# Kernel tuning notes

Hardware: AMD Instinct MI355X
Metric: run time of the kernel (lower is better)

## Reference

```python
import jax, jax.numpy as jnp
import numpy as np


def setup_inputs() -> dict:
    key = jax.random.key(0)
    ks = jax.random.split(key, 8)
    B, H, W = 4, 1024, 1024
    F_, Nuv = 40000, 25000
    Ht, Wt = 1024, 1024
    # pytorch3d-style globally packed face indices: pixel of batch b holds idx in [b*F, (b+1)*F) or -1
    local = jax.random.randint(ks[0], (B, H, W, 1), 0, F_)
    covered = jax.random.uniform(ks[1], (B, H, W, 1)) < 0.8
    offset = (jnp.arange(B) * F_)[:, None, None, None]
    pix_to_face = jnp.where(covered, local + offset, -1).astype(jnp.int64)
    bary = jax.random.uniform(ks[2], (B, H, W, 1, 3), dtype=jnp.float32)
    bary = bary / jnp.sum(bary, axis=-1, keepdims=True)
    uvmap = jax.random.normal(ks[3], (B, 3, Ht, Wt), dtype=jnp.float32)
    vertex_uv = jax.random.uniform(ks[4], (Nuv, 2), dtype=jnp.float32)
    face_uv = jax.random.randint(ks[5], (F_, 3), 0, Nuv).astype(jnp.int64)
    bkg_color = jnp.zeros((3,), jnp.float32)
    return {"bary_coords": bary, "uvmap": uvmap, "vertex_uv": vertex_uv,
            "bkg_color": bkg_color, "pix_to_face": pix_to_face,
            "face_uv": face_uv, "num_faces": F_}


def _bilinear_sample(tex, u, v):
    # tex: [B,C,Ht,Wt]; u,v: [B,H,W] in pixel coords (align_corners=True), border padding
    B, C, Ht, Wt = tex.shape
    u = jnp.clip(u, 0.0, Wt - 1.0)
    v = jnp.clip(v, 0.0, Ht - 1.0)
    x0 = jnp.floor(u)
    y0 = jnp.floor(v)
    x0i = x0.astype(jnp.int32)
    y0i = y0.astype(jnp.int32)
    x1i = jnp.minimum(x0i + 1, Wt - 1)
    y1i = jnp.minimum(y0i + 1, Ht - 1)
    wx = (u - x0)[..., None]
    wy = (v - y0)[..., None]
    bidx = jnp.arange(B)[:, None, None]
    g = lambda yi, xi: tex[bidx, :, yi, xi]  # [B,H,W,C]
    top = g(y0i, x0i) * (1.0 - wx) + g(y0i, x1i) * wx
    bot = g(y1i, x0i) * (1.0 - wx) + g(y1i, x1i) * wx
    return top * (1.0 - wy) + bot * wy  # [B,H,W,C]


def reference(bary_coords, uvmap, vertex_uv, bkg_color, pix_to_face, face_uv, num_faces):
    B, H, W, K = pix_to_face.shape
    Ht, Wt = uvmap.shape[2], uvmap.shape[3]
    # vertex_uv with v flipped, as in forward(): stack((u, 1-v))
    vt = jnp.stack([vertex_uv[:, 0], 1.0 - vertex_uv[:, 1]], axis=1)  # [Nuv,2]
    face_vt = vt[face_uv]  # [F,3,2]
    pf = pix_to_face[..., 0]  # [B,H,W] globally packed indices
    valid = pf != -1
    # unpack global -> per-batch local face index (invalid pixels -> 0, masked later)
    local = jnp.where(valid, pf - jnp.arange(B, dtype=pf.dtype)[:, None, None] * num_faces, 0)
    uv_tri = face_vt[local]  # [B,H,W,3,2]
    # barycentric interpolation of the 3 vertex uvs
    uv = jnp.einsum('bhwk,bhwkc->bhwc', bary_coords[:, :, :, 0, :], uv_tri)  # [B,H,W,2]
    sampled = _bilinear_sample(uvmap, uv[..., 0] * (Wt - 1), uv[..., 1] * (Ht - 1))  # [B,H,W,3]
    render = jnp.transpose(sampled, (0, 3, 1, 2))  # [B,3,H,W]
    is_valid = valid[:, None, :, :].astype(render.dtype)  # [B,1,H,W]
    render = render * is_valid + bkg_color[None, :, None, None] * (1.0 - is_valid)
    return render, is_valid
```

## Files before the change

### kernel.cpp

```cpp
#include <hip/hip_runtime.h>
#include <hip/hip_fp16.h>


#define BB   4
#define HWT  (1 << 20)
#define WMASK 1023

static __device__ __forceinline__ unsigned h2b(float a, float b) {
    __half2 h = __floats2half2_rn(a, b);
    return *reinterpret_cast<const unsigned*>(&h);
}
static __device__ __forceinline__ float2 h2f(unsigned u) {
    return __half22float2(*reinterpret_cast<const __half2*>(&u));
}

__global__ __launch_bounds__(256) void build_ftab(
    const int* __restrict__ face_uv, const float* __restrict__ vertex_uv,
    float4* __restrict__ ftab, int F)
{
    const int f = blockIdx.x * blockDim.x + threadIdx.x;
    if (f >= F) return;
    const int i0 = face_uv[f * 3 + 0];
    const int i1 = face_uv[f * 3 + 1];
    const int i2 = face_uv[f * 3 + 2];
    float4 a, b;
    a.x = vertex_uv[i0 * 2 + 0]; a.y = 1.0f - vertex_uv[i0 * 2 + 1];
    a.z = vertex_uv[i1 * 2 + 0]; a.w = 1.0f - vertex_uv[i1 * 2 + 1];
    b.x = vertex_uv[i2 * 2 + 0]; b.y = 1.0f - vertex_uv[i2 * 2 + 1];
    b.z = 0.0f; b.w = 0.0f;
    ftab[f * 2 + 0] = a;
    ftab[f * 2 + 1] = b;
}

template <bool PAD32>
__global__ __launch_bounds__(256) void pack_quad(
    const float* __restrict__ uvmap, unsigned* __restrict__ ptexu)
{
    const int i = blockIdx.x * blockDim.x + threadIdx.x;
    const int b  = i >> 20;
    const int hw = i & (HWT - 1);
    const int x  = hw & WMASK;
    const int y  = hw >> 10;
    const int xr = min(x + 1, WMASK);
    const int yd = min(y + 1, WMASK);
    const float* base = uvmap + ((size_t)b * 3 << 20);
    const int iTL = (y  << 10) | x,  iTR = (y  << 10) | xr;
    const int iBL = (yd << 10) | x,  iBR = (yd << 10) | xr;
    const float c0TL = base[iTL],           c0TR = base[iTR];
    const float c1TL = base[HWT + iTL],     c1TR = base[HWT + iTR];
    const float c2TL = base[2 * HWT + iTL], c2TR = base[2 * HWT + iTR];
    const float c0BL = base[iBL],           c0BR = base[iBR];
    const float c1BL = base[HWT + iBL],     c1BR = base[HWT + iBR];
    const float c2BL = base[2 * HWT + iBL], c2BR = base[2 * HWT + iBR];

    const unsigned t0 = h2b(c0TL, c1TL), t1 = h2b(c2TL, c0TR), t2 = h2b(c1TR, c2TR);
    const unsigned u0 = h2b(c0BL, c1BL), u1 = h2b(c2BL, c0BR), u2 = h2b(c1BR, c2BR);

    if (PAD32) {
        uint4* p = reinterpret_cast<uint4*>(ptexu);
        uint4 a; a.x = t0; a.y = t1; a.z = t2; a.w = 0u;
        uint4 c; c.x = u0; c.y = u1; c.z = u2; c.w = 0u;
        p[(size_t)i * 2 + 0] = a;
        p[(size_t)i * 2 + 1] = c;
    } else {
        const size_t o = (size_t)i * 6;
        ptexu[o + 0] = t0; ptexu[o + 1] = t1; ptexu[o + 2] = t2;
        ptexu[o + 3] = u0; ptexu[o + 4] = u1; ptexu[o + 5] = u2;
    }
}

template <bool PAD32>
__global__ __launch_bounds__(256) void render_quad(
    const unsigned* __restrict__ ptexu, const float4* __restrict__ ftab,
    const float* __restrict__ bary, const int* __restrict__ pix,
    const float* __restrict__ bkg, int F,
    float* __restrict__ render, float* __restrict__ is_valid)
{
    const int tid = blockIdx.x * blockDim.x + threadIdx.x;
    const float bkg0 = bkg[0], bkg1 = bkg[1], bkg2 = bkg[2];

    int pf[4];
    #pragma unroll
    for (int j = 0; j < 4; ++j)
        pf[j] = __builtin_nontemporal_load(&pix[(j << 20) | tid]);

    float ba[4][3];
    #pragma unroll
    for (int j = 0; j < 4; ++j) {
        const size_t o = (size_t)((j << 20) | tid) * 3;
        ba[j][0] = __builtin_nontemporal_load(&bary[o + 0]);
        ba[j][1] = __builtin_nontemporal_load(&bary[o + 1]);
        ba[j][2] = __builtin_nontemporal_load(&bary[o + 2]);
    }

    float4 A[4], Bv[4];
    #pragma unroll
    for (int j = 0; j < 4; ++j) {
        const int lf = (pf[j] != -1) ? pf[j] - j * F : 0;
        A[j]  = ftab[lf * 2 + 0];
        Bv[j] = ftab[lf * 2 + 1];
    }

    unsigned t0[4], t1[4], t2[4], u0[4], u1[4], u2[4];
    float wx[4], wy[4];
    #pragma unroll
    for (int j = 0; j < 4; ++j) {
        const float u = ba[j][0] * A[j].x + ba[j][1] * A[j].z + ba[j][2] * Bv[j].x;
        const float v = ba[j][0] * A[j].y + ba[j][1] * A[j].w + ba[j][2] * Bv[j].y;
        float x = fminf(fmaxf(u * 1023.0f, 0.0f), 1023.0f);
        float y = fminf(fmaxf(v * 1023.0f, 0.0f), 1023.0f);
        if (pf[j] == -1) { x = 0.0f; y = 0.0f; }
        const float xf = floorf(x), yf = floorf(y);
        wx[j] = x - xf; wy[j] = y - yf;
        const int e = (j << 20) | (((int)yf) << 10) | (int)xf;
        if (PAD32) {
            const uint4* p = reinterpret_cast<const uint4*>(ptexu);
            const uint4 qt = p[(size_t)e * 2 + 0];
            const uint4 qb = p[(size_t)e * 2 + 1];
            t0[j] = qt.x; t1[j] = qt.y; t2[j] = qt.z;
            u0[j] = qb.x; u1[j] = qb.y; u2[j] = qb.z;
        } else {
            const size_t o = (size_t)e * 6;
            t0[j] = ptexu[o + 0]; t1[j] = ptexu[o + 1]; t2[j] = ptexu[o + 2];
            u0[j] = ptexu[o + 3]; u1[j] = ptexu[o + 4]; u2[j] = ptexu[o + 5];
        }
    }

    #pragma unroll
    for (int j = 0; j < 4; ++j) {
        const float2 a01 = h2f(t0[j]), a2b = h2f(t1[j]), a12 = h2f(t2[j]);
        const float2 c01 = h2f(u0[j]), c2b = h2f(u1[j]), c12 = h2f(u2[j]);
        const float iwx = 1.0f - wx[j], iwy = 1.0f - wy[j];
        const float top0 = a01.x * iwx + a2b.y * wx[j];
        const float top1 = a01.y * iwx + a12.x * wx[j];
        const float top2 = a2b.x * iwx + a12.y * wx[j];
        const float bot0 = c01.x * iwx + c2b.y * wx[j];
        const float bot1 = c01.y * iwx + c12.x * wx[j];
        const float bot2 = c2b.x * iwx + c12.y * wx[j];
        float r0 = top0 * iwy + bot0 * wy[j];
        float r1 = top1 * iwy + bot1 * wy[j];
        float r2 = top2 * iwy + bot2 * wy[j];
        float vf = 1.0f;
        if (pf[j] == -1) { r0 = bkg0; r1 = bkg1; r2 = bkg2; vf = 0.0f; }
        const int ob = (j * 3) << 20;
        __builtin_nontemporal_store(r0, &render[ob | tid]);
        __builtin_nontemporal_store(r1, &render[(ob + HWT) | tid]);
        __builtin_nontemporal_store(r2, &render[(ob + 2 * HWT) | tid]);
        __builtin_nontemporal_store(vf, &is_valid[(j << 20) | tid]);
    }
}

__global__ __launch_bounds__(256) void uvrender_direct(
    const float* __restrict__ bary, const float* __restrict__ uvmap,
    const float* __restrict__ vertex_uv, const float* __restrict__ bkg,
    const int* __restrict__ pix_to_face, const int* __restrict__ face_uv,
    int F, float* __restrict__ render, float* __restrict__ is_valid)
{
    const int total = BB * HWT;
    const float bkg0 = bkg[0], bkg1 = bkg[1], bkg2 = bkg[2];
    for (int idx = blockIdx.x * blockDim.x + threadIdx.x; idx < total;
         idx += gridDim.x * blockDim.x) {
        const int b  = idx >> 20;
        const int hw = idx & (HWT - 1);
        const int pf = pix_to_face[idx];
        float r0 = bkg0, r1 = bkg1, r2 = bkg2, vflag = 0.0f;
        if (pf != -1) {
            vflag = 1.0f;
            const int local = pf - b * F;
            const int i0 = face_uv[local * 3 + 0];
            const int i1 = face_uv[local * 3 + 1];
            const int i2 = face_uv[local * 3 + 2];
            const float b0 = bary[(size_t)idx * 3 + 0];
            const float b1 = bary[(size_t)idx * 3 + 1];
            const float b2 = bary[(size_t)idx * 3 + 2];
            const float u = b0 * vertex_uv[i0 * 2] + b1 * vertex_uv[i1 * 2] +
                            b2 * vertex_uv[i2 * 2];
            const float v = b0 * (1.0f - vertex_uv[i0 * 2 + 1]) +
                            b1 * (1.0f - vertex_uv[i1 * 2 + 1]) +
                            b2 * (1.0f - vertex_uv[i2 * 2 + 1]);
            float x = fminf(fmaxf(u * 1023.0f, 0.0f), 1023.0f);
            float y = fminf(fmaxf(v * 1023.0f, 0.0f), 1023.0f);
            const float xf = floorf(x), yf = floorf(y);
            const int x0 = (int)xf, y0 = (int)yf;
            const int x1 = min(x0 + 1, WMASK), y1 = min(y0 + 1, WMASK);
            const float wx = x - xf, wy = y - yf;
            const float iwx = 1.0f - wx, iwy = 1.0f - wy;
            const float* texb = uvmap + ((size_t)b * 3 << 20);
            float out[3];
            #pragma unroll
            for (int c = 0; c < 3; ++c) {
                const float* t = texb + ((size_t)c << 20);
                const float t00 = t[(y0 << 10) | x0];
                const float t01 = t[(y0 << 10) | x1];
                const float t10 = t[(y1 << 10) | x0];
                const float t11 = t[(y1 << 10) | x1];
                out[c] = (t00 * iwx + t01 * wx) * iwy + (t10 * iwx + t11 * wx) * wy;
            }
            r0 = out[0]; r1 = out[1]; r2 = out[2];
        }
        const size_t ob = (size_t)b * 3 * HWT + hw;
        __builtin_nontemporal_store(r0, &render[ob]);
        __builtin_nontemporal_store(r1, &render[ob + HWT]);
        __builtin_nontemporal_store(r2, &render[ob + 2 * (size_t)HWT]);
        __builtin_nontemporal_store(vflag, &is_valid[idx]);
    }
}

extern "C" void kernel_launch(void* const* d_in, const int* in_sizes, int n_in,
                              void* d_out, int out_size, void* d_ws, size_t ws_size,
                              hipStream_t stream) {
    const float* bary        = (const float*)d_in[0];
    const float* uvmap       = (const float*)d_in[1];
    const float* vertex_uv   = (const float*)d_in[2];
    const float* bkg         = (const float*)d_in[3];
    const int*   pix_to_face = (const int*)d_in[4];
    const int*   face_uv     = (const int*)d_in[5];
    const int F = in_sizes[5] / 3;

    float* render   = (float*)d_out;
    float* is_valid = (float*)d_out + (size_t)BB * 3 * HWT;

    const size_t Q32_B  = (size_t)BB * HWT * 32;
    const size_t Q24_B  = (size_t)BB * HWT * 24;
    const size_t FTAB_B = (size_t)F * 2 * sizeof(float4);

    if (ws_size >= Q32_B + FTAB_B) {
        unsigned* ptexu = (unsigned*)d_ws;
        float4*   ftab  = (float4*)((char*)d_ws + Q32_B);
        build_ftab<<<(F + 255) / 256, 256, 0, stream>>>(face_uv, vertex_uv, ftab, F);
        pack_quad<true><<<(BB * HWT) / 256, 256, 0, stream>>>(uvmap, ptexu);
        render_quad<true><<<HWT / 256, 256, 0, stream>>>(
            ptexu, ftab, bary, pix_to_face, bkg, F, render, is_valid);
    } else if (ws_size >= Q24_B + FTAB_B) {
        unsigned* ptexu = (unsigned*)d_ws;
        float4*   ftab  = (float4*)((char*)d_ws + Q24_B);
        build_ftab<<<(F + 255) / 256, 256, 0, stream>>>(face_uv, vertex_uv, ftab, F);
        pack_quad<false><<<(BB * HWT) / 256, 256, 0, stream>>>(uvmap, ptexu);
        render_quad<false><<<HWT / 256, 256, 0, stream>>>(
            ptexu, ftab, bary, pix_to_face, bkg, F, render, is_valid);
    } else {
        uvrender_direct<<<2048, 256, 0, stream>>>(
            bary, uvmap, vertex_uv, bkg, pix_to_face, face_uv, F,
            render, is_valid);
    }
}
```

Measured before the change: 137.7 us.

## Interleave texture packing and rendering in two batch-pair chunks for cache locality

Splits the pack and render kernels so that each pair of batches is packed and then immediately rendered, alternating in two rounds. This is meant to keep the freshly written packed quad texture for the current batches resident in the last-level cache while the render gathers read it, instead of writing all four batches before any reads. Render threads now cover two batches at two half-image offsets rather than four batches at one offset. The cost is two extra kernel launches and serialisation between chunks.

New measurement: 138.9 us. About the same (+0.9%).

```diff
diff --git a/kernel.cpp b/kernel.cpp
--- a/kernel.cpp
+++ b/kernel.cpp
@@ -2,9 +2,10 @@
 #include <hip/hip_fp16.h>
 
 
-#define BB   4
-#define HWT  (1 << 20)
+#define BB    4
+#define HWT   (1 << 20)
 #define WMASK 1023
+#define HHALF (HWT / 2)
 
 static __device__ __forceinline__ unsigned h2b(float a, float b) {
     __half2 h = __floats2half2_rn(a, b);
@@ -33,12 +34,13 @@
 }
 
 template <bool PAD32>
-__global__ __launch_bounds__(256) void pack_quad(
-    const float* __restrict__ uvmap, unsigned* __restrict__ ptexu)
-{
-    const int i = blockIdx.x * blockDim.x + threadIdx.x;
-    const int b  = i >> 20;
-    const int hw = i & (HWT - 1);
+__global__ __launch_bounds__(256) void pack_quad_chunk(
+    const float* __restrict__ uvmap, unsigned* __restrict__ ptexu, int b0)
+{
+    const int t = blockIdx.x * blockDim.x + threadIdx.x;
+    const int b  = b0 + (t >> 20);
+    const int hw = t & (HWT - 1);
+    const int i  = (b << 20) | hw;
     const int x  = hw & WMASK;
     const int y  = hw >> 10;
     const int xr = min(x + 1, WMASK);
@@ -70,24 +72,31 @@
 }
 
 template <bool PAD32>
-__global__ __launch_bounds__(256) void render_quad(
+__global__ __launch_bounds__(256) void render_chunk(
     const unsigned* __restrict__ ptexu, const float4* __restrict__ ftab,
     const float* __restrict__ bary, const int* __restrict__ pix,
     const float* __restrict__ bkg, int F,
-    float* __restrict__ render, float* __restrict__ is_valid)
+    float* __restrict__ render, float* __restrict__ is_valid, int b0)
 {
     const int tid = blockIdx.x * blockDim.x + threadIdx.x;
     const float bkg0 = bkg[0], bkg1 = bkg[1], bkg2 = bkg[2];
 
+    int idx[4], bj[4];
+    #pragma unroll
+    for (int j = 0; j < 4; ++j) {
+        bj[j]  = b0 + (j >> 1);
+        idx[j] = (bj[j] << 20) | (tid + ((j & 1) ? HHALF : 0));
+    }
+
     int pf[4];
     #pragma unroll
     for (int j = 0; j < 4; ++j)
-        pf[j] = __builtin_nontemporal_load(&pix[(j << 20) | tid]);
+        pf[j] = __builtin_nontemporal_load(&pix[idx[j]]);
 
     float ba[4][3];
     #pragma unroll
     for (int j = 0; j < 4; ++j) {
-        const size_t o = (size_t)((j << 20) | tid) * 3;
+        const size_t o = (size_t)idx[j] * 3;
         ba[j][0] = __builtin_nontemporal_load(&bary[o + 0]);
         ba[j][1] = __builtin_nontemporal_load(&bary[o + 1]);
         ba[j][2] = __builtin_nontemporal_load(&bary[o + 2]);
@@ -96,7 +105,7 @@
     float4 A[4], Bv[4];
     #pragma unroll
     for (int j = 0; j < 4; ++j) {
-        const int lf = (pf[j] != -1) ? pf[j] - j * F : 0;
+        const int lf = (pf[j] != -1) ? pf[j] - bj[j] * F : 0;
         A[j]  = ftab[lf * 2 + 0];
         Bv[j] = ftab[lf * 2 + 1];
     }
@@ -112,7 +121,7 @@
         if (pf[j] == -1) { x = 0.0f; y = 0.0f; }
         const float xf = floorf(x), yf = floorf(y);
         wx[j] = x - xf; wy[j] = y - yf;
-        const int e = (j << 20) | (((int)yf) << 10) | (int)xf;
+        const int e = (bj[j] << 20) | (((int)yf) << 10) | (int)xf;
         if (PAD32) {
             const uint4* p = reinterpret_cast<const uint4*>(ptexu);
             const uint4 qt = p[(size_t)e * 2 + 0];
@@ -142,11 +151,12 @@
         float r2 = top2 * iwy + bot2 * wy[j];
         float vf = 1.0f;
         if (pf[j] == -1) { r0 = bkg0; r1 = bkg1; r2 = bkg2; vf = 0.0f; }
-        const int ob = (j * 3) << 20;
-        __builtin_nontemporal_store(r0, &render[ob | tid]);
-        __builtin_nontemporal_store(r1, &render[(ob + HWT) | tid]);
-        __builtin_nontemporal_store(r2, &render[(ob + 2 * HWT) | tid]);
-        __builtin_nontemporal_store(vf, &is_valid[(j << 20) | tid]);
+        const int hwj = idx[j] & (HWT - 1);
+        const int ob  = (bj[j] * 3) << 20;
+        __builtin_nontemporal_store(r0, &render[ob + hwj]);
+        __builtin_nontemporal_store(r1, &render[ob + HWT + hwj]);
+        __builtin_nontemporal_store(r2, &render[ob + 2 * HWT + hwj]);
+        __builtin_nontemporal_store(vf, &is_valid[idx[j]]);
     }
 }
 
@@ -183,8 +193,8 @@
             const float xf = floorf(x), yf = floorf(y);
             const int x0 = (int)xf, y0 = (int)yf;
             const int x1 = min(x0 + 1, WMASK), y1 = min(y0 + 1, WMASK);
-            const float wx = x - xf, wy = y - yf;
-            const float iwx = 1.0f - wx, iwy = 1.0f - wy;
+            const float wxx = x - xf, wyy = y - yf;
+            const float iwx = 1.0f - wxx, iwy = 1.0f - wyy;
             const float* texb = uvmap + ((size_t)b * 3 << 20);
             float out[3];
             #pragma unroll
@@ -194,7 +204,7 @@
                 const float t01 = t[(y0 << 10) | x1];
                 const float t10 = t[(y1 << 10) | x0];
                 const float t11 = t[(y1 << 10) | x1];
-                out[c] = (t00 * iwx + t01 * wx) * iwy + (t10 * iwx + t11 * wx) * wy;
+                out[c] = (t00 * iwx + t01 * wxx) * iwy + (t10 * iwx + t11 * wxx) * wyy;
             }
             r0 = out[0]; r1 = out[1]; r2 = out[2];
         }
@@ -228,16 +238,20 @@
         unsigned* ptexu = (unsigned*)d_ws;
         float4*   ftab  = (float4*)((char*)d_ws + Q32_B);
         build_ftab<<<(F + 255) / 256, 256, 0, stream>>>(face_uv, vertex_uv, ftab, F);
-        pack_quad<true><<<(BB * HWT) / 256, 256, 0, stream>>>(uvmap, ptexu);
-        render_quad<true><<<HWT / 256, 256, 0, stream>>>(
-            ptexu, ftab, bary, pix_to_face, bkg, F, render, is_valid);
+        for (int c = 0; c < 2; ++c) {
+            pack_quad_chunk<true><<<(2 * HWT) / 256, 256, 0, stream>>>(uvmap, ptexu, c * 2);
+            render_chunk<true><<<HHALF / 256, 256, 0, stream>>>(
+                ptexu, ftab, bary, pix_to_face, bkg, F, render, is_valid, c * 2);
+        }
     } else if (ws_size >= Q24_B + FTAB_B) {
         unsigned* ptexu = (unsigned*)d_ws;
         float4*   ftab  = (float4*)((char*)d_ws + Q24_B);
         build_ftab<<<(F + 255) / 256, 256, 0, stream>>>(face_uv, vertex_uv, ftab, F);
-        pack_quad<false><<<(BB * HWT) / 256, 256, 0, stream>>>(uvmap, ptexu);
-        render_quad<false><<<HWT / 256, 256, 0, stream>>>(
-            ptexu, ftab, bary, pix_to_face, bkg, F, render, is_valid);
+        for (int c = 0; c < 2; ++c) {
+            pack_quad_chunk<false><<<(2 * HWT) / 256, 256, 0, stream>>>(uvmap, ptexu, c * 2);
+            render_chunk<false><<<HHALF / 256, 256, 0, stream>>>(
+                ptexu, ftab, bary, pix_to_face, bkg, F, render, is_valid, c * 2);
+        }
     } else {
         uvrender_direct<<<2048, 256, 0, stream>>>(
             bary, uvmap, vertex_uv, bkg, pix_to_face, face_uv, F,
```
